# Kernel optimization log

Measured on AMD Instinct MI355X. Metric: run time of the kernel, lower is better.

## Reference

```python
import jax, jax.numpy as jnp
import numpy as np

B, T, F_IN, H = 512, 512, 64, 128
BN_EPS = 1e-3  # Keras BatchNormalization default epsilon


def setup_inputs() -> dict:
    key = jax.random.key(0)
    ks = jax.random.split(key, 12)
    x = jax.random.normal(ks[0], (B, T, F_IN), dtype=jnp.float32)
    # last channel is a discrete phase index in {0,1,2}, stored as float
    state = jax.random.randint(ks[1], (B, T, 1), 0, 3).astype(jnp.float32)
    inputs = jnp.concatenate([x, state], axis=-1)  # [B, T, F_IN+1]
    s = 1.0 / np.sqrt(H)
    return {
        "inputs": inputs,
        "Wx": jax.random.normal(ks[2], (F_IN, 3 * H), dtype=jnp.float32) * s,
        "Wh": jax.random.normal(ks[3], (H, 3 * H), dtype=jnp.float32) * s,
        "b": jax.random.normal(ks[4], (2, 3 * H), dtype=jnp.float32) * 0.01,
        "W_state": jax.random.normal(ks[5], (3, H), dtype=jnp.float32),
        "w1": jax.random.normal(ks[6], (H, 64), dtype=jnp.float32) * s,
        "b1": jnp.zeros((64,), jnp.float32),
        "gamma": jnp.ones((64,), jnp.float32),
        "beta": jnp.zeros((64,), jnp.float32),
        "mean": jnp.zeros((64,), jnp.float32),
        "var": jnp.ones((64,), jnp.float32),
        "w2": jax.random.normal(ks[7], (64, 1), dtype=jnp.float32) * 0.125,
        "b2": jnp.zeros((1,), jnp.float32),
    }


def _gru_final_state(x, Wx, Wh, b):
    # Keras GRU, reset_after=True (default): separate input / recurrent biases.
    b_in, b_rec = b[0], b[1]
    xw = x @ Wx + b_in                      # [B, T, 3H] (precompute input matmuls)
    xw_t = jnp.swapaxes(xw, 0, 1)           # [T, B, 3H]
    h0 = jnp.zeros((x.shape[0], Wh.shape[0]), x.dtype)

    def step(h, xw_step):
        rec = h @ Wh + b_rec                # [B, 3H]
        xz, xr, xh = jnp.split(xw_step, 3, axis=-1)
        rz, rr, rh = jnp.split(rec, 3, axis=-1)
        z = jax.nn.sigmoid(xz + rz)
        r = jax.nn.sigmoid(xr + rr)
        hh = jnp.tanh(xh + r * rh)
        h_new = z * h + (1.0 - z) * hh
        return h_new, None

    h_final, _ = jax.lax.scan(step, h0, xw_t)
    return h_final                          # [B, H]


def reference(inputs, Wx, Wh, b, W_state, w1, b1, gamma, beta, mean, var, w2, b2):
    x = inputs[:, :, :-1]                   # [B, T, F_IN]
    state = inputs[:, :, -1]                # [B, T]
    hidden = _gru_final_state(x, Wx, Wh, b)  # [B, H]
    idx = jnp.clip(state[:, -1].astype(jnp.int32), 0, W_state.shape[0] - 1)
    hidden = hidden + W_state[idx]          # gather-add phase effect
    h = jax.nn.relu(hidden @ w1 + b1)       # dense1
    # dropout: identity in inference mode
    h = (h - mean) * jax.lax.rsqrt(var + BN_EPS) * gamma + beta  # batchnorm (inference)
    return h @ w2 + b2                      # [B, 1]
```

## Files before the change

### kernel.cpp

```cpp
#include <hip/hip_runtime.h>
#include <hip/hip_bf16.h>

#define T_SEQ   512
#define H_DIM   128
#define N3H     384
#define HSW     128
#define XS      72

typedef float f32x4 __attribute__((ext_vector_type(4)));
typedef float f32x2 __attribute__((ext_vector_type(2)));
typedef __bf16 bf16x8 __attribute__((ext_vector_type(8)));
typedef unsigned short us8 __attribute__((ext_vector_type(8)));

static __device__ __forceinline__ unsigned short f2bf(float f) {
    unsigned int u = __builtin_bit_cast(unsigned int, f);
    u += 0x7FFFu + ((u >> 16) & 1u);
    return (unsigned short)(u >> 16);
}

static __device__ __forceinline__ unsigned cvt_pk_bf16(float a, float b) {
    unsigned r;
    asm("v_cvt_pk_bf16_f32 %0, %1, %2" : "=v"(r) : "v"(a), "v"(b));
    return r;
}

static __device__ __forceinline__ void lds_barrier() {
    asm volatile("" ::: "memory");
    __builtin_amdgcn_s_waitcnt(0xC07F);
    __builtin_amdgcn_s_barrier();
    asm volatile("" ::: "memory");
}

static __device__ __forceinline__ bf16x8 ld8(const unsigned short* p) {
    return __builtin_bit_cast(bf16x8, *(const us8*)p);
}

__global__ __launch_bounds__(512, 1) void gru_fused(
    const float* __restrict__ inputs, const float* __restrict__ Wx,
    const float* __restrict__ Wh, const float* __restrict__ bias,
    const float* __restrict__ W_state, const float* __restrict__ w1,
    const float* __restrict__ b1, const float* __restrict__ gamma,
    const float* __restrict__ beta, const float* __restrict__ mean,
    const float* __restrict__ var, const float* __restrict__ w2,
    const float* __restrict__ b2, float* __restrict__ out)
{
    __shared__ __attribute__((aligned(16))) unsigned short hb[2][16 * HSW];
    __shared__ __attribute__((aligned(16))) unsigned short xb[2][16 * XS];
    __shared__ float hf[16][H_DIM + 1];

    const int tid  = threadIdx.x;
    const int w    = tid >> 6;
    const int lane = tid & 63;
    const int m    = lane & 15;
    const int q    = lane >> 4;
    const int b0   = blockIdx.x * 16;

    const float SCL0 = -1.4426950408889634f;
    const float SCL2 =  2.8853900817779268f;

    bf16x8 whB[3][4];
    bf16x8 wxB[3][2];
    f32x4 xinit[3];
    f32x4 rinit2;
    const f32x4 zero4 = { 0.f, 0.f, 0.f, 0.f };
#pragma unroll
    for (int g = 0; g < 3; ++g) {
        const float s = (g < 2) ? SCL0 : SCL2;
        const int col = (8 * g + w) * 16 + m;
#pragma unroll
        for (int k = 0; k < 4; ++k) {
            us8 tmp;
#pragma unroll
            for (int j = 0; j < 8; ++j) tmp[j] = f2bf(s * Wh[(32 * k + 8 * q + j) * N3H + col]);
            whB[g][k] = __builtin_bit_cast(bf16x8, tmp);
        }
#pragma unroll
        for (int k = 0; k < 2; ++k) {
            us8 tmp;
#pragma unroll
            for (int j = 0; j < 8; ++j) tmp[j] = f2bf(s * Wx[(32 * k + 8 * q + j) * N3H + col]);
            wxB[g][k] = __builtin_bit_cast(bf16x8, tmp);
        }
        const float bi = s * bias[col];
        const float br = s * bias[N3H + col];
        if (g < 2) {
            const float bc = bi + br;
            xinit[g] = (f32x4){ bc, bc, bc, bc };
        } else {
            xinit[g] = (f32x4){ bi, bi, bi, bi };
            rinit2   = (f32x4){ br, br, br, br };
        }
    }

    int hro[4], hwo[4], xro[2];
#pragma unroll
    for (int k = 0; k < 4; ++k) hro[k] = m * HSW + (((4 * k + q) ^ (m & 7)) * 8);
#pragma unroll
    for (int i = 0; i < 4; ++i) {
        const int row = 4 * q + i;
        hwo[i] = row * HSW + (((2 * w + (m >> 3)) ^ (row & 7)) * 8) + (m & 7);
    }
#pragma unroll
    for (int k = 0; k < 2; ++k) xro[k] = m * XS + 32 * k + 8 * q;

    const int sr = tid >> 5;
    const int c2 = (tid & 31) * 2;
    const int xwoff = sr * XS + c2;
    const float* xs = inputs + ((size_t)(b0 + sr) * T_SEQ) * 65 + c2;

    {
        unsigned int* p = (unsigned int*)hb[0];
        for (int i = tid; i < 16 * HSW / 2; i += 512) p[i] = 0;
    }
    *(unsigned*)&xb[0][xwoff] = cvt_pk_bf16(xs[0], xs[1]);
    *(unsigned*)&xb[1][xwoff] = cvt_pk_bf16(xs[65], xs[66]);
    lds_barrier();

    f32x4 xwA[3], xwB[3];
    {
        bf16x8 xa[2];
#pragma unroll
        for (int k = 0; k < 2; ++k) xa[k] = ld8(&xb[0][xro[k]]);
#pragma unroll
        for (int g = 0; g < 3; ++g) {
            f32x4 acc = __builtin_amdgcn_mfma_f32_16x16x32_bf16(xa[0], wxB[g][0], xinit[g], 0, 0, 0);
            acc = __builtin_amdgcn_mfma_f32_16x16x32_bf16(xa[1], wxB[g][1], acc, 0, 0, 0);
            xwA[g] = acc;
        }
    }

    float pf0a = xs[2 * 65], pf0b = xs[2 * 65 + 1];
    float pf1a = 0.f, pf1b = 0.f;

    f32x4 hreg = { 0.f, 0.f, 0.f, 0.f };

    auto step = [&](int t, f32x4* xw_cur, f32x4* xw_next,
                    float& pfLa, float& pfLb, float pfUa, float pfUb,
                    const unsigned short* hcur, unsigned short* hnxt,
                    const unsigned short* xnxt, unsigned short* xwr) {
        if (t <= T_SEQ - 4) { pfLa = xs[(t + 3) * 65]; pfLb = xs[(t + 3) * 65 + 1]; }

        lds_barrier();

        bf16x8 ha[4];
#pragma unroll
        for (int k = 0; k < 4; ++k) ha[k] = ld8(&hcur[hro[k]]);
        bf16x8 xa[2];
        if (t < T_SEQ - 1) {
#pragma unroll
            for (int k = 0; k < 2; ++k) xa[k] = ld8(&xnxt[xro[k]]);
        }

        f32x4 racc[3];
#pragma unroll
        for (int g = 0; g < 3; ++g) {
            f32x4 acc = __builtin_amdgcn_mfma_f32_16x16x32_bf16(ha[0], whB[g][0], (g == 2) ? rinit2 : zero4, 0, 0, 0);
            acc = __builtin_amdgcn_mfma_f32_16x16x32_bf16(ha[1], whB[g][1], acc, 0, 0, 0);
            acc = __builtin_amdgcn_mfma_f32_16x16x32_bf16(ha[2], whB[g][2], acc, 0, 0, 0);
            acc = __builtin_amdgcn_mfma_f32_16x16x32_bf16(ha[3], whB[g][3], acc, 0, 0, 0);
            racc[g] = acc;
        }

        f32x4 az = xw_cur[0] + racc[0];
        f32x4 ar = xw_cur[1] + racc[1];
        f32x4 ea, eb;
#pragma unroll
        for (int i = 0; i < 4; ++i) { ea[i] = __builtin_amdgcn_exp2f(az[i]); eb[i] = __builtin_amdgcn_exp2f(ar[i]); }
        f32x4 Pa = ea + 1.0f;
        f32x4 Pb = eb + 1.0f;
        f32x4 PP = Pa * Pb;
        f32x4 D;
#pragma unroll
        for (int i = 0; i < 4; ++i) D[i] = __builtin_amdgcn_rcpf(PP[i]);
        f32x4 z = Pb * D;
        f32x4 r = Pa * D;
        f32x4 u = r * racc[2] + xw_cur[2];
        f32x4 ec;
#pragma unroll
        for (int i = 0; i < 4; ++i) ec[i] = __builtin_amdgcn_exp2f(u[i]);
        f32x4 Pc = ec + 1.0f;
        f32x4 rc;
#pragma unroll
        for (int i = 0; i < 4; ++i) rc[i] = __builtin_amdgcn_rcpf(Pc[i]);
        f32x4 hh = -2.0f * rc + 1.0f;
        f32x4 hnew = z * (hreg - hh) + hh;
        hreg = hnew;

        if (t < T_SEQ - 1) {
#pragma unroll
            for (int g = 0; g < 3; ++g) {
                f32x4 acc = __builtin_amdgcn_mfma_f32_16x16x32_bf16(xa[0], wxB[g][0], xinit[g], 0, 0, 0);
                acc = __builtin_amdgcn_mfma_f32_16x16x32_bf16(xa[1], wxB[g][1], acc, 0, 0, 0);
                xw_next[g] = acc;
            }
        }

        {
            const unsigned p01 = cvt_pk_bf16(hnew[0], hnew[1]);
            const unsigned p23 = cvt_pk_bf16(hnew[2], hnew[3]);
            hnxt[hwo[0]] = (unsigned short)(p01);
            hnxt[hwo[1]] = (unsigned short)(p01 >> 16);
            hnxt[hwo[2]] = (unsigned short)(p23);
            hnxt[hwo[3]] = (unsigned short)(p23 >> 16);
        }

        if (t <= T_SEQ - 3) *(unsigned*)&xwr[xwoff] = cvt_pk_bf16(pfUa, pfUb);
    };

    for (int t = 0; t < T_SEQ; t += 2) {
        step(t,     xwA, xwB, pf1a, pf1b, pf0a, pf0b, hb[0], hb[1], xb[1], xb[0]);
        step(t + 1, xwB, xwA, pf0a, pf0b, pf1a, pf1b, hb[1], hb[0], xb[0], xb[1]);
    }

#pragma unroll
    for (int i = 0; i < 4; ++i)
        hf[4 * q + i][16 * w + m] = hreg[i];
    __syncthreads();

    {
        const int row = tid >> 5;
        const int c0  = (tid & 31) * 4;
        const float sf = inputs[((size_t)(b0 + row) * T_SEQ + (T_SEQ - 1)) * 65 + 64];
        int si = (int)sf;
        si = si < 0 ? 0 : (si > 2 ? 2 : si);
#pragma unroll
        for (int c = 0; c < 4; ++c)
            hf[row][c0 + c] += W_state[si * H_DIM + c0 + c];
    }
    __syncthreads();

    {
        const int row = tid >> 5;
        const int jj  = (tid & 31) * 2;
        f32x2 acc = { b1[jj], b1[jj + 1] };
        for (int k = 0; k < H_DIM; ++k) {
            const float hv = hf[row][k];
            const f32x2 wv = *(const f32x2*)(w1 + k * 64 + jj);
            acc[0] = fmaf(hv, wv[0], acc[0]);
            acc[1] = fmaf(hv, wv[1], acc[1]);
        }
        float v = 0.0f;
#pragma unroll
        for (int ii = 0; ii < 2; ++ii) {
            const int j = jj + ii;
            float a = fmaxf(acc[ii], 0.0f);
            a = (a - mean[j]) * rsqrtf(var[j] + 1e-3f) * gamma[j] + beta[j];
            v = fmaf(a, w2[j], v);
        }
        v += __shfl_down(v, 16);
        v += __shfl_down(v, 8);
        v += __shfl_down(v, 4);
        v += __shfl_down(v, 2);
        v += __shfl_down(v, 1);
        if ((tid & 31) == 0) out[b0 + row] = v + b2[0];
    }
}

extern "C" void kernel_launch(void* const* d_in, const int* in_sizes, int n_in,
                              void* d_out, int out_size, void* d_ws, size_t ws_size,
                              hipStream_t stream) {
    (void)in_sizes; (void)n_in; (void)out_size; (void)d_ws; (void)ws_size;
    const float* inputs  = (const float*)d_in[0];
    const float* Wx      = (const float*)d_in[1];
    const float* Wh      = (const float*)d_in[2];
    const float* bias    = (const float*)d_in[3];
    const float* W_state = (const float*)d_in[4];
    const float* w1      = (const float*)d_in[5];
    const float* b1      = (const float*)d_in[6];
    const float* gamma   = (const float*)d_in[7];
    const float* beta    = (const float*)d_in[8];
    const float* mean    = (const float*)d_in[9];
    const float* var     = (const float*)d_in[10];
    const float* w2      = (const float*)d_in[11];
    const float* b2      = (const float*)d_in[12];
    float* out = (float*)d_out;

    gru_fused<<<32, 512, 0, stream>>>(inputs, Wx, Wh, bias, W_state, w1, b1,
                                      gamma, beta, mean, var, w2, b2, out);
}
```

Before: 422.5 us.

## Split input projection into a parallel prepass kernel before the recurrence

```diff
diff --git a/kernel.cpp b/kernel.cpp
--- a/kernel.cpp
+++ b/kernel.cpp
@@ -9,8 +9,10 @@
 
 typedef float f32x4 __attribute__((ext_vector_type(4)));
 typedef float f32x2 __attribute__((ext_vector_type(2)));
+typedef float f32x4u __attribute__((ext_vector_type(4), aligned(4)));
 typedef __bf16 bf16x8 __attribute__((ext_vector_type(8)));
 typedef unsigned short us8 __attribute__((ext_vector_type(8)));
+typedef unsigned int u32x2 __attribute__((ext_vector_type(2)));
 
 static __device__ __forceinline__ unsigned short f2bf(float f) {
     unsigned int u = __builtin_bit_cast(unsigned int, f);
@@ -35,7 +37,254 @@
     return __builtin_bit_cast(bf16x8, *(const us8*)p);
 }
 
-__global__ __launch_bounds__(512, 1) void gru_fused(
+__global__ __launch_bounds__(512, 1) void xw_prepass(
+    const float* __restrict__ inputs, const float* __restrict__ Wx,
+    const float* __restrict__ bias, float* __restrict__ xw)
+{
+    __shared__ __attribute__((aligned(16))) unsigned short xl[16][16 * XS];
+
+    const int tid  = threadIdx.x;
+    const int w    = tid >> 6;
+    const int lane = tid & 63;
+    const int m    = lane & 15;
+    const int q    = lane >> 4;
+    const int b_blk = blockIdx.x & 31;
+    const int t0    = (blockIdx.x >> 5) * 16;
+    const int b0    = b_blk * 16;
+
+    const float SCL0 = -1.4426950408889634f;
+    const float SCL2 =  2.8853900817779268f;
+
+    bf16x8 wxB[3][2];
+    f32x4 xinit[3];
+#pragma unroll
+    for (int g = 0; g < 3; ++g) {
+        const float s = (g < 2) ? SCL0 : SCL2;
+        const int col = (8 * g + w) * 16 + m;
+#pragma unroll
+        for (int k = 0; k < 2; ++k) {
+            us8 tmp;
+#pragma unroll
+            for (int j = 0; j < 8; ++j) tmp[j] = f2bf(s * Wx[(32 * k + 8 * q + j) * N3H + col]);
+            wxB[g][k] = __builtin_bit_cast(bf16x8, tmp);
+        }
+        const float bi = s * bias[col];
+        const float br = s * bias[N3H + col];
+        const float bc = (g < 2) ? (bi + br) : bi;
+        xinit[g] = (f32x4){ bc, bc, bc, bc };
+    }
+
+    int xro[2];
+#pragma unroll
+    for (int k = 0; k < 2; ++k) xro[k] = m * XS + 32 * k + 8 * q;
+
+    {
+        const int tt   = tid & 15;
+        const int r    = (tid >> 4) & 15;
+        const int half = tid >> 8;
+        const float* src = inputs + ((size_t)(b0 + r) * T_SEQ + (t0 + tt)) * 65 + half * 32;
+        unsigned short* dst = &xl[tt][r * XS + half * 32];
+#pragma unroll
+        for (int j = 0; j < 8; ++j) {
+            f32x4u v = *(const f32x4u*)(src + 4 * j);
+            u32x2 pk;
+            pk[0] = cvt_pk_bf16(v[0], v[1]);
+            pk[1] = cvt_pk_bf16(v[2], v[3]);
+            *(u32x2*)(dst + 4 * j) = pk;
+        }
+    }
+    __syncthreads();
+
+    for (int tt = 0; tt < 16; ++tt) {
+        bf16x8 xa[2];
+#pragma unroll
+        for (int k = 0; k < 2; ++k) xa[k] = ld8(&xl[tt][xro[k]]);
+        float* outp = xw + ((size_t)(b_blk * 512 + t0 + tt) * 24 + w * 3) * 256 + lane * 4;
+#pragma unroll
+        for (int g = 0; g < 3; ++g) {
+            f32x4 acc = __builtin_amdgcn_mfma_f32_16x16x32_bf16(xa[0], wxB[g][0], xinit[g], 0, 0, 0);
+            acc = __builtin_amdgcn_mfma_f32_16x16x32_bf16(xa[1], wxB[g][1], acc, 0, 0, 0);
+            *(f32x4*)(outp + g * 256) = acc;
+        }
+    }
+}
+
+__global__ __launch_bounds__(512, 1) void gru_rec(
+    const float* __restrict__ inputs, const float* __restrict__ Wh,
+    const float* __restrict__ bias, const float* __restrict__ xw,
+    const float* __restrict__ W_state, const float* __restrict__ w1,
+    const float* __restrict__ b1, const float* __restrict__ gamma,
+    const float* __restrict__ beta, const float* __restrict__ mean,
+    const float* __restrict__ var, const float* __restrict__ w2,
+    const float* __restrict__ b2, float* __restrict__ out)
+{
+    __shared__ __attribute__((aligned(16))) unsigned short hb[2][16 * HSW];
+    __shared__ float hf[16][H_DIM + 1];
+
+    const int tid  = threadIdx.x;
+    const int w    = tid >> 6;
+    const int lane = tid & 63;
+    const int m    = lane & 15;
+    const int q    = lane >> 4;
+    const int bI   = blockIdx.x;
+    const int b0   = bI * 16;
+
+    const float SCL0 = -1.4426950408889634f;
+    const float SCL2 =  2.8853900817779268f;
+
+    bf16x8 whB[3][4];
+    f32x4 rinit2;
+    const f32x4 zero4 = { 0.f, 0.f, 0.f, 0.f };
+#pragma unroll
+    for (int g = 0; g < 3; ++g) {
+        const float s = (g < 2) ? SCL0 : SCL2;
+        const int col = (8 * g + w) * 16 + m;
+#pragma unroll
+        for (int k = 0; k < 4; ++k) {
+            us8 tmp;
+#pragma unroll
+            for (int j = 0; j < 8; ++j) tmp[j] = f2bf(s * Wh[(32 * k + 8 * q + j) * N3H + col]);
+            whB[g][k] = __builtin_bit_cast(bf16x8, tmp);
+        }
+        if (g == 2) {
+            const float br = s * bias[N3H + col];
+            rinit2 = (f32x4){ br, br, br, br };
+        }
+    }
+
+    int hro[4], hwo[4];
+#pragma unroll
+    for (int k = 0; k < 4; ++k) hro[k] = m * HSW + (((4 * k + q) ^ (m & 7)) * 8);
+#pragma unroll
+    for (int i = 0; i < 4; ++i) {
+        const int row = 4 * q + i;
+        hwo[i] = row * HSW + (((2 * w + (m >> 3)) ^ (row & 7)) * 8) + (m & 7);
+    }
+
+    {
+        unsigned int* p = (unsigned int*)hb[0];
+        for (int i = tid; i < 16 * HSW / 2; i += 512) p[i] = 0;
+    }
+
+    const float* xwp = xw + ((size_t)bI * 512 * 24 + w * 3) * 256 + lane * 4;
+    f32x4 xwA[3], xwB[3];
+#pragma unroll
+    for (int g = 0; g < 3; ++g) xwA[g] = *(const f32x4u*)(xwp + g * 256);
+    xwp += 24 * 256;
+
+    f32x4 hreg = { 0.f, 0.f, 0.f, 0.f };
+
+    auto step = [&](int t, f32x4* cur, f32x4* nxt,
+                    const unsigned short* hcur, unsigned short* hnxt) {
+        if (t < T_SEQ - 1) {
+#pragma unroll
+            for (int g = 0; g < 3; ++g) nxt[g] = *(const f32x4u*)(xwp + g * 256);
+            xwp += 24 * 256;
+        }
+
+        lds_barrier();
+
+        bf16x8 ha[4];
+#pragma unroll
+        for (int k = 0; k < 4; ++k) ha[k] = ld8(&hcur[hro[k]]);
+
+        __builtin_amdgcn_s_setprio(1);
+        f32x4 racc[3];
+#pragma unroll
+        for (int g = 0; g < 3; ++g) {
+            f32x4 acc = __builtin_amdgcn_mfma_f32_16x16x32_bf16(ha[0], whB[g][0], (g == 2) ? rinit2 : zero4, 0, 0, 0);
+            acc = __builtin_amdgcn_mfma_f32_16x16x32_bf16(ha[1], whB[g][1], acc, 0, 0, 0);
+            acc = __builtin_amdgcn_mfma_f32_16x16x32_bf16(ha[2], whB[g][2], acc, 0, 0, 0);
+            acc = __builtin_amdgcn_mfma_f32_16x16x32_bf16(ha[3], whB[g][3], acc, 0, 0, 0);
+            racc[g] = acc;
+        }
+        __builtin_amdgcn_s_setprio(0);
+
+        f32x4 az = cur[0] + racc[0];
+        f32x4 ar = cur[1] + racc[1];
+        f32x4 ea, eb;
+#pragma unroll
+        for (int i = 0; i < 4; ++i) { ea[i] = __builtin_amdgcn_exp2f(az[i]); eb[i] = __builtin_amdgcn_exp2f(ar[i]); }
+        f32x4 Pa = ea + 1.0f;
+        f32x4 Pb = eb + 1.0f;
+        f32x4 PP = Pa * Pb;
+        f32x4 D;
+#pragma unroll
+        for (int i = 0; i < 4; ++i) D[i] = __builtin_amdgcn_rcpf(PP[i]);
+        f32x4 z = Pb * D;
+        f32x4 r = Pa * D;
+        f32x4 u = r * racc[2] + cur[2];
+        f32x4 ec;
+#pragma unroll
+        for (int i = 0; i < 4; ++i) ec[i] = __builtin_amdgcn_exp2f(u[i]);
+        f32x4 Pc = ec + 1.0f;
+        f32x4 rc;
+#pragma unroll
+        for (int i = 0; i < 4; ++i) rc[i] = __builtin_amdgcn_rcpf(Pc[i]);
+        f32x4 hh = -2.0f * rc + 1.0f;
+        f32x4 hnew = z * (hreg - hh) + hh;
+        hreg = hnew;
+
+        {
+            const unsigned p01 = cvt_pk_bf16(hnew[0], hnew[1]);
+            const unsigned p23 = cvt_pk_bf16(hnew[2], hnew[3]);
+            hnxt[hwo[0]] = (unsigned short)(p01);
+            hnxt[hwo[1]] = (unsigned short)(p01 >> 16);
+            hnxt[hwo[2]] = (unsigned short)(p23);
+            hnxt[hwo[3]] = (unsigned short)(p23 >> 16);
+        }
+    };
+
+    for (int t = 0; t < T_SEQ; t += 2) {
+        step(t,     xwA, xwB, hb[0], hb[1]);
+        step(t + 1, xwB, xwA, hb[1], hb[0]);
+    }
+
+#pragma unroll
+    for (int i = 0; i < 4; ++i)
+        hf[4 * q + i][16 * w + m] = hreg[i];
+    __syncthreads();
+
+    {
+        const int row = tid >> 5;
+        const int c0  = (tid & 31) * 4;
+        const float sf = inputs[((size_t)(b0 + row) * T_SEQ + (T_SEQ - 1)) * 65 + 64];
+        int si = (int)sf;
+        si = si < 0 ? 0 : (si > 2 ? 2 : si);
+#pragma unroll
+        for (int c = 0; c < 4; ++c)
+            hf[row][c0 + c] += W_state[si * H_DIM + c0 + c];
+    }
+    __syncthreads();
+
+    {
+        const int row = tid >> 5;
+        const int jj  = (tid & 31) * 2;
+        f32x2 acc = { b1[jj], b1[jj + 1] };
+        for (int k = 0; k < H_DIM; ++k) {
+            const float hv = hf[row][k];
+            const f32x2 wv = *(const f32x2*)(w1 + k * 64 + jj);
+            acc[0] = fmaf(hv, wv[0], acc[0]);
+            acc[1] = fmaf(hv, wv[1], acc[1]);
+        }
+        float v = 0.0f;
+#pragma unroll
+        for (int ii = 0; ii < 2; ++ii) {
+            const int j = jj + ii;
+            float a = fmaxf(acc[ii], 0.0f);
+            a = (a - mean[j]) * rsqrtf(var[j] + 1e-3f) * gamma[j] + beta[j];
+            v = fmaf(a, w2[j], v);
+        }
+        v += __shfl_down(v, 16);
+        v += __shfl_down(v, 8);
+        v += __shfl_down(v, 4);
+        v += __shfl_down(v, 2);
+        v += __shfl_down(v, 1);
+        if ((tid & 31) == 0) out[b0 + row] = v + b2[0];
+    }
+}
+
+__global__ __launch_bounds__(512, 1) void gru_fused_legacy(
     const float* __restrict__ inputs, const float* __restrict__ Wx,
     const float* __restrict__ Wh, const float* __restrict__ bias,
     const float* __restrict__ W_state, const float* __restrict__ w1,
@@ -259,7 +508,7 @@
 extern "C" void kernel_launch(void* const* d_in, const int* in_sizes, int n_in,
                               void* d_out, int out_size, void* d_ws, size_t ws_size,
                               hipStream_t stream) {
-    (void)in_sizes; (void)n_in; (void)out_size; (void)d_ws; (void)ws_size;
+    (void)in_sizes; (void)n_in; (void)out_size;
     const float* inputs  = (const float*)d_in[0];
     const float* Wx      = (const float*)d_in[1];
     const float* Wh      = (const float*)d_in[2];
@@ -275,6 +524,15 @@
     const float* b2      = (const float*)d_in[12];
     float* out = (float*)d_out;
 
-    gru_fused<<<32, 512, 0, stream>>>(inputs, Wx, Wh, bias, W_state, w1, b1,
-                                      gamma, beta, mean, var, w2, b2, out);
-}
+    const size_t XW_BYTES = (size_t)512 * T_SEQ * N3H * sizeof(float);
+    if (d_ws != nullptr && ws_size >= XW_BYTES) {
+        float* xw = (float*)d_ws;
+        xw_prepass<<<1024, 512, 0, stream>>>(inputs, Wx, bias, xw);
+        gru_rec<<<32, 512, 0, stream>>>(inputs, Wh, bias, xw, W_state, w1, b1,
+                                        gamma, beta, mean, var, w2, b2, out);
+    } else {
+        gru_fused_legacy<<<32, 512, 0, stream>>>(inputs, Wx, Wh, bias, W_state,
+                                                 w1, b1, gamma, beta, mean, var,
+                                                 w2, b2, out);
+    }
+}
```

New measurement: 421.6 us. About the same (-0.2%).
